# Optimization experiments

Hardware: AMD Instinct MI355X
Metric: run time of the kernel (lower is better)

The kernel has to match this reference:

```python
import jax, jax.numpy as jnp
import numpy as np
import math

IN_F, OUT_F = 512, 512
N_HEADS, N_SPLITS = 32, 4
N = 1024
DELTA_SCALE = 0.1


def setup_inputs() -> dict:
    key = jax.random.key(0)
    k_x, k_h, k_s, k_w = jax.random.split(key, 4)
    stdv = 1.0 / math.sqrt(OUT_F)
    inputs = {
        "input": jax.random.normal(k_x, (N, IN_F), dtype=jnp.float32),
        "head_ix": jax.random.randint(k_h, (N,), 0, N_HEADS, dtype=jnp.int32),
        "split_ix": jax.random.randint(k_s, (N,), 0, N_SPLITS, dtype=jnp.int32),
        # learned parameters (EmbeddingTensor tables)
        "weight": jax.random.uniform(k_w, (N_HEADS, IN_F, OUT_F), dtype=jnp.float32,
                                     minval=-stdv, maxval=stdv),
        "delta_weight": jnp.zeros((N_HEADS * N_SPLITS, IN_F, OUT_F), dtype=jnp.float32),
        "bias": jnp.zeros((N_HEADS, OUT_F), dtype=jnp.float32),
    }
    return inputs


def reference(input, head_ix, split_ix, weight, delta_weight, bias):
    # per-sample weight: base[head] + 0.1 * delta[head * n_splits + split]
    w = weight[head_ix] + delta_weight[head_ix * N_SPLITS + split_ix] * DELTA_SCALE  # [N, in, out]
    # batched vector-matrix multiply + per-head bias
    return jnp.einsum('ab,abc->ac', input, w) + bias[head_ix]  # [N, out]
```

## Files before the change

### kernel.cpp

```cpp
#include <hip/hip_runtime.h>

#define N_SAMP   1024
#define IN_F     512
#define OUT_F    512
#define N_HEADS  32
#define N_SPLITS 4
#define N_GROUPS (N_HEADS * N_SPLITS)
#define DELTA_SCALE 0.1f

#define KSPLIT   8
#define KROWS    (IN_F / KSPLIT)
#define JC       16


__global__ __launch_bounds__(256, 4) void lms_partial(
    const float* __restrict__ X, const int* __restrict__ head_ix,
    const int* __restrict__ split_ix, const float* __restrict__ W,
    const float* __restrict__ D, float* __restrict__ ws)
{
    __shared__ float Xs[JC][KROWS];
    __shared__ int   list[N_SAMP];
    __shared__ int   wsum[4];

    const int b       = blockIdx.x;
    const int logical = (b & 7) * 128 + (b >> 3);
    const int g       = logical >> 3;
    const int kb      = logical & 7;
    const int h       = g >> 2;

    const int tid  = threadIdx.x;
    const int lane = tid & 63;
    const int wave = tid >> 6;

    int run = 0;
    for (int r = 0; r < N_SAMP / 256; ++r) {
        const int i   = r * 256 + tid;
        const int key = head_ix[i] * N_SPLITS + split_ix[i];
        const bool hit = (key == g);
        const unsigned long long m = __ballot(hit);
        if (lane == 0) wsum[wave] = __popcll(m);
        __syncthreads();
        int base = run;
        for (int w = 0; w < 4; ++w)
            if (w < wave) base += wsum[w];
        if (hit)
            list[base + __popcll(m & ((1ULL << lane) - 1ULL))] = i;
        run += wsum[0] + wsum[1] + wsum[2] + wsum[3];
        __syncthreads();
    }
    const int total = run;
    if (total == 0) return;

    const float* wq = W + (size_t)h * (IN_F * OUT_F)
                    + (size_t)(kb * KROWS) * OUT_F + 2 * tid;
    const float* dq = D + (size_t)g * (IN_F * OUT_F)
                    + (size_t)(kb * KROWS) * OUT_F + 2 * tid;

    for (int cb = 0; cb < total; cb += JC) {
        const int nc = min(total - cb, JC);

        __syncthreads();
        {
            const int s  = tid >> 4;
            const int qq = tid & 15;
            float4 v = make_float4(0.f, 0.f, 0.f, 0.f);
            if (s < nc)
                v = *(const float4*)(X + (size_t)list[cb + s] * IN_F
                                     + kb * KROWS + qq * 4);
            *(float4*)(&Xs[s][qq * 4]) = v;
        }
        __syncthreads();

        float2 acc[JC];
#pragma unroll
        for (int j = 0; j < JC; ++j) { acc[j].x = 0.f; acc[j].y = 0.f; }

        float2 wr[2][4], dr[2][4];
#pragma unroll
        for (int f = 0; f < 4; ++f) {
            wr[0][f] = *(const float2*)(wq + (size_t)f * OUT_F);
            dr[0][f] = *(const float2*)(dq + (size_t)f * OUT_F);
        }

        constexpr int NB = KROWS / 4;
#pragma unroll 2
        for (int bt = 0; bt < NB; ++bt) {
            const int cur = bt & 1, nxt = cur ^ 1;
            const int nr = (bt + 1 < NB) ? (bt + 1) * 4 : bt * 4;
#pragma unroll
            for (int f = 0; f < 4; ++f) {
                wr[nxt][f] = *(const float2*)(wq + (size_t)(nr + f) * OUT_F);
                dr[nxt][f] = *(const float2*)(dq + (size_t)(nr + f) * OUT_F);
            }

            float2 rc[4];
#pragma unroll
            for (int f = 0; f < 4; ++f) {
                rc[f].x = wr[cur][f].x + DELTA_SCALE * dr[cur][f].x;
                rc[f].y = wr[cur][f].y + DELTA_SCALE * dr[cur][f].y;
            }

#pragma unroll
            for (int j = 0; j < JC; ++j) {
                const float4 xv = *(const float4*)(&Xs[j][bt * 4]);
                acc[j].x += xv.x * rc[0].x; acc[j].y += xv.x * rc[0].y;
                acc[j].x += xv.y * rc[1].x; acc[j].y += xv.y * rc[1].y;
                acc[j].x += xv.z * rc[2].x; acc[j].y += xv.z * rc[2].y;
                acc[j].x += xv.w * rc[3].x; acc[j].y += xv.w * rc[3].y;
            }
        }

#pragma unroll
        for (int j = 0; j < JC; ++j) {
            if (j < nc) {
                float* op = ws + ((size_t)kb * N_SAMP + list[cb + j]) * OUT_F
                          + 2 * tid;
                *(float2*)op = acc[j];
            }
        }
    }
}

__global__ __launch_bounds__(256, 4) void lms_reduce(
    const float* __restrict__ ws, const int* __restrict__ head_ix,
    const float* __restrict__ bias, float* __restrict__ out)
{
    const int gid = blockIdx.x * 256 + threadIdx.x;
    const int i   = gid >> 7;
    const int c4  = gid & 127;
    const int h   = head_ix[i];

    float4 s = *(const float4*)(bias + (size_t)h * OUT_F + 4 * c4);
#pragma unroll
    for (int kb = 0; kb < KSPLIT; ++kb) {
        const float4 p = *(const float4*)(ws + ((size_t)kb * N_SAMP + i) * OUT_F
                                          + 4 * c4);
        s.x += p.x; s.y += p.y; s.z += p.z; s.w += p.w;
    }
    *(float4*)(out + (size_t)i * OUT_F + 4 * c4) = s;
}

__global__ __launch_bounds__(256, 4) void lms_fused(
    const float* __restrict__ X, const int* __restrict__ head_ix,
    const int* __restrict__ split_ix, const float* __restrict__ W,
    const float* __restrict__ D, const float* __restrict__ bias,
    float* __restrict__ out)
{
    constexpr int J    = 16;
    constexpr int KQ   = 8;
    constexpr int KT   = IN_F / KQ;
    constexpr int NST  = KT / 4;
    constexpr int NOUT = (J * 32) / 256;

    __shared__ float buf[J * IN_F];
    __shared__ int   list[N_SAMP];
    __shared__ int   wsum[4];

    const int g    = blockIdx.y;
    const int h    = g >> 2;
    const int c0   = blockIdx.x * 64;
    const int tid  = threadIdx.x;
    const int c2   = tid & 31;
    const int kq   = tid >> 5;
    const int lane = tid & 63;
    const int wave = tid >> 6;

    int run = 0;
    for (int r = 0; r < N_SAMP / 256; ++r) {
        const int i   = r * 256 + tid;
        const int key = head_ix[i] * N_SPLITS + split_ix[i];
        const bool hit = (key == g);
        const unsigned long long m = __ballot(hit);
        if (lane == 0) wsum[wave] = __popcll(m);
        __syncthreads();
        int base = run;
        for (int w = 0; w < 4; ++w)
            if (w < wave) base += wsum[w];
        if (hit)
            list[base + __popcll(m & ((1ULL << lane) - 1ULL))] = i;
        run += wsum[0] + wsum[1] + wsum[2] + wsum[3];
        __syncthreads();
    }
    const int total = run;
    if (total == 0) return;

    const size_t roff = (size_t)(kq * KT) * OUT_F + c0 + c2 * 2;
    const float* wp = W + (size_t)h * (IN_F * OUT_F) + roff;
    const float* dp = D + (size_t)g * (IN_F * OUT_F) + roff;

    for (int s0 = 0; s0 < total; s0 += J) {
        const int nc = min(total - s0, J);
        __syncthreads();
        for (int i = tid; i < J * (IN_F / 4); i += 256) {
            const int s = i >> 7, q = i & 127;
            float4 v = make_float4(0.f, 0.f, 0.f, 0.f);
            if (s < nc)
                v = *(const float4*)(X + (size_t)list[s0 + s] * IN_F + q * 4);
            *(float4*)(&buf[s * IN_F + q * 4]) = v;
        }
        __syncthreads();

        float2 acc[J];
#pragma unroll
        for (int j = 0; j < J; ++j) { acc[j].x = 0.f; acc[j].y = 0.f; }

        float2 wb[2][4], db[2][4];
#pragma unroll
        for (int u = 0; u < 4; ++u) {
            wb[0][u] = *(const float2*)(wp + (size_t)u * OUT_F);
            db[0][u] = *(const float2*)(dp + (size_t)u * OUT_F);
        }

#pragma unroll 2
        for (int st = 0; st < NST; ++st) {
            const int nx = (st + 1 < NST) ? st + 1 : NST - 1;
            const int nb = (st + 1) & 1, cb = st & 1;
            const float* wn = wp + (size_t)(nx * 4) * OUT_F;
            const float* dn = dp + (size_t)(nx * 4) * OUT_F;
#pragma unroll
            for (int u = 0; u < 4; ++u) {
                wb[nb][u] = *(const float2*)(wn + (size_t)u * OUT_F);
                db[nb][u] = *(const float2*)(dn + (size_t)u * OUT_F);
            }
            float2 rc[4];
#pragma unroll
            for (int u = 0; u < 4; ++u) {
                rc[u].x = wb[cb][u].x + DELTA_SCALE * db[cb][u].x;
                rc[u].y = wb[cb][u].y + DELTA_SCALE * db[cb][u].y;
            }
            const float* xb = &buf[kq * KT + st * 4];
#pragma unroll
            for (int j = 0; j < J; ++j) {
                const float4 xv = *(const float4*)(xb + j * IN_F);
                acc[j].x += xv.x * rc[0].x; acc[j].y += xv.x * rc[0].y;
                acc[j].x += xv.y * rc[1].x; acc[j].y += xv.y * rc[1].y;
                acc[j].x += xv.z * rc[2].x; acc[j].y += xv.z * rc[2].y;
                acc[j].x += xv.w * rc[3].x; acc[j].y += xv.w * rc[3].y;
            }
        }

        __syncthreads();
        float2* Red = (float2*)buf;
#pragma unroll
        for (int j = 0; j < J; ++j)
            Red[(kq * J + j) * 32 + c2] = acc[j];
        __syncthreads();

#pragma unroll
        for (int t = 0; t < NOUT; ++t) {
            const int oi = t * 256 + tid;
            const int j = oi >> 5, cc = oi & 31;
            if (j < nc) {
                float2 s = make_float2(0.f, 0.f);
#pragma unroll
                for (int q = 0; q < KQ; ++q) {
                    const float2 r = Red[(q * J + j) * 32 + cc];
                    s.x += r.x; s.y += r.y;
                }
                const float2 bv =
                    *(const float2*)(bias + (size_t)h * OUT_F + c0 + cc * 2);
                float* op = out + (size_t)list[s0 + j] * OUT_F + c0 + cc * 2;
                float2 res;
                res.x = s.x + bv.x;
                res.y = s.y + bv.y;
                *(float2*)op = res;
            }
        }
    }
}

extern "C" void kernel_launch(void* const* d_in, const int* in_sizes, int n_in,
                              void* d_out, int out_size, void* d_ws, size_t ws_size,
                              hipStream_t stream) {
    const float* X        = (const float*)d_in[0];
    const int*   head_ix  = (const int*)d_in[1];
    const int*   split_ix = (const int*)d_in[2];
    const float* W        = (const float*)d_in[3];
    const float* D        = (const float*)d_in[4];
    const float* bias     = (const float*)d_in[5];
    float*       out      = (float*)d_out;

    const size_t ws_need = (size_t)KSPLIT * N_SAMP * OUT_F * sizeof(float);
    if (ws_size >= ws_need) {
        float* ws = (float*)d_ws;
        lms_partial<<<dim3(N_GROUPS * KSPLIT), 256, 0, stream>>>(
            X, head_ix, split_ix, W, D, ws);
        lms_reduce<<<dim3((N_SAMP * OUT_F / 4) / 256), 256, 0, stream>>>(
            ws, head_ix, bias, out);
    } else {
        dim3 gf(OUT_F / 64, N_GROUPS);
        lms_fused<<<gf, 256, 0, stream>>>(X, head_ix, split_ix, W, D, bias, out);
    }
}
```

Baseline: 269.2 us.

## Widen per-thread output tile to float4 and split K across half-blocks

The partial kernel now has each thread compute four output columns with float4 weight and delta loads. The two halves of a block each cover 64 K rows of a 128-row chunk, so the grid shrinks to 512 blocks. Block indices are remapped so that heads sharing the same K chunk are interleaved, which may improve locality of the base weight in L2. The aim is wider loads and more reuse of each X value from shared memory, at the cost of more registers (launch bounds lowered to 2 blocks per SM) and fewer blocks to hide latency.

Measured after the change: 254.0 us. 1.06x faster.

```diff
diff --git a/kernel.cpp b/kernel.cpp
--- a/kernel.cpp
+++ b/kernel.cpp
@@ -8,27 +8,33 @@
 #define N_GROUPS (N_HEADS * N_SPLITS)
 #define DELTA_SCALE 0.1f
 
-#define KSPLIT   8
-#define KROWS    (IN_F / KSPLIT)
+#define NKB      4
+#define KR2      128
+#define KRH      64
+#define NPLANES  8
 #define JC       16
 
 
-__global__ __launch_bounds__(256, 4) void lms_partial(
+__global__ __launch_bounds__(256, 2) void lms_partial4(
     const float* __restrict__ X, const int* __restrict__ head_ix,
     const int* __restrict__ split_ix, const float* __restrict__ W,
     const float* __restrict__ D, float* __restrict__ ws)
 {
-    __shared__ float Xs[JC][KROWS];
+    __shared__ float Xs[JC][KR2];
     __shared__ int   list[N_SAMP];
     __shared__ int   wsum[4];
 
-    const int b       = blockIdx.x;
-    const int logical = (b & 7) * 128 + (b >> 3);
-    const int g       = logical >> 3;
-    const int kb      = logical & 7;
-    const int h       = g >> 2;
+    const int b   = blockIdx.x;
+    const int x   = b & 7;
+    const int j5  = b >> 3;
+    const int h   = x | ((j5 & 3) << 3);
+    const int s   = (j5 >> 2) & 3;
+    const int kb  = j5 >> 4;
+    const int g   = h * N_SPLITS + s;
 
     const int tid  = threadIdx.x;
+    const int c4   = tid & 127;
+    const int kh   = tid >> 7;
     const int lane = tid & 63;
     const int wave = tid >> 6;
 
@@ -51,71 +57,81 @@
     const int total = run;
     if (total == 0) return;
 
+    const int krow0 = kb * KR2 + kh * KRH;
     const float* wq = W + (size_t)h * (IN_F * OUT_F)
-                    + (size_t)(kb * KROWS) * OUT_F + 2 * tid;
+                    + (size_t)krow0 * OUT_F + 4 * c4;
     const float* dq = D + (size_t)g * (IN_F * OUT_F)
-                    + (size_t)(kb * KROWS) * OUT_F + 2 * tid;
+                    + (size_t)krow0 * OUT_F + 4 * c4;
+    const int plane = kb * 2 + kh;
 
     for (int cb = 0; cb < total; cb += JC) {
         const int nc = min(total - cb, JC);
 
         __syncthreads();
-        {
-            const int s  = tid >> 4;
-            const int qq = tid & 15;
+        for (int f = 0; f < 2; ++f) {
+            const int fid = f * 256 + tid;
+            const int ss = fid >> 5, qq = fid & 31;
             float4 v = make_float4(0.f, 0.f, 0.f, 0.f);
-            if (s < nc)
-                v = *(const float4*)(X + (size_t)list[cb + s] * IN_F
-                                     + kb * KROWS + qq * 4);
-            *(float4*)(&Xs[s][qq * 4]) = v;
-        }
-        __syncthreads();
-
-        float2 acc[JC];
-#pragma unroll
-        for (int j = 0; j < JC; ++j) { acc[j].x = 0.f; acc[j].y = 0.f; }
-
-        float2 wr[2][4], dr[2][4];
+            if (ss < nc)
+                v = *(const float4*)(X + (size_t)list[cb + ss] * IN_F
+                                     + kb * KR2 + qq * 4);
+            *(float4*)(&Xs[ss][qq * 4]) = v;
+        }
+        __syncthreads();
+
+        float4 acc[JC];
+#pragma unroll
+        for (int j = 0; j < JC; ++j)
+            acc[j] = make_float4(0.f, 0.f, 0.f, 0.f);
+
+        float4 wr[2][4], dr[2][4];
 #pragma unroll
         for (int f = 0; f < 4; ++f) {
-            wr[0][f] = *(const float2*)(wq + (size_t)f * OUT_F);
-            dr[0][f] = *(const float2*)(dq + (size_t)f * OUT_F);
-        }
-
-        constexpr int NB = KROWS / 4;
+            wr[0][f] = *(const float4*)(wq + (size_t)f * OUT_F);
+            dr[0][f] = *(const float4*)(dq + (size_t)f * OUT_F);
+        }
+
+        constexpr int NB = KRH / 4;
 #pragma unroll 2
         for (int bt = 0; bt < NB; ++bt) {
             const int cur = bt & 1, nxt = cur ^ 1;
             const int nr = (bt + 1 < NB) ? (bt + 1) * 4 : bt * 4;
 #pragma unroll
             for (int f = 0; f < 4; ++f) {
-                wr[nxt][f] = *(const float2*)(wq + (size_t)(nr + f) * OUT_F);
-                dr[nxt][f] = *(const float2*)(dq + (size_t)(nr + f) * OUT_F);
-            }
-
-            float2 rc[4];
+                wr[nxt][f] = *(const float4*)(wq + (size_t)(nr + f) * OUT_F);
+                dr[nxt][f] = *(const float4*)(dq + (size_t)(nr + f) * OUT_F);
+            }
+
+            float4 rc[4];
 #pragma unroll
             for (int f = 0; f < 4; ++f) {
                 rc[f].x = wr[cur][f].x + DELTA_SCALE * dr[cur][f].x;
                 rc[f].y = wr[cur][f].y + DELTA_SCALE * dr[cur][f].y;
+                rc[f].z = wr[cur][f].z + DELTA_SCALE * dr[cur][f].z;
+                rc[f].w = wr[cur][f].w + DELTA_SCALE * dr[cur][f].w;
             }
 
 #pragma unroll
             for (int j = 0; j < JC; ++j) {
-                const float4 xv = *(const float4*)(&Xs[j][bt * 4]);
+                const float4 xv =
+                    *(const float4*)(&Xs[j][kh * KRH + bt * 4]);
                 acc[j].x += xv.x * rc[0].x; acc[j].y += xv.x * rc[0].y;
+                acc[j].z += xv.x * rc[0].z; acc[j].w += xv.x * rc[0].w;
                 acc[j].x += xv.y * rc[1].x; acc[j].y += xv.y * rc[1].y;
+                acc[j].z += xv.y * rc[1].z; acc[j].w += xv.y * rc[1].w;
                 acc[j].x += xv.z * rc[2].x; acc[j].y += xv.z * rc[2].y;
+                acc[j].z += xv.z * rc[2].z; acc[j].w += xv.z * rc[2].w;
                 acc[j].x += xv.w * rc[3].x; acc[j].y += xv.w * rc[3].y;
+                acc[j].z += xv.w * rc[3].z; acc[j].w += xv.w * rc[3].w;
             }
         }
 
 #pragma unroll
         for (int j = 0; j < JC; ++j) {
             if (j < nc) {
-                float* op = ws + ((size_t)kb * N_SAMP + list[cb + j]) * OUT_F
-                          + 2 * tid;
-                *(float2*)op = acc[j];
+                float* op = ws + ((size_t)plane * N_SAMP + list[cb + j]) * OUT_F
+                          + 4 * c4;
+                *(float4*)op = acc[j];
             }
         }
     }
@@ -132,10 +148,10 @@
 
     float4 s = *(const float4*)(bias + (size_t)h * OUT_F + 4 * c4);
 #pragma unroll
-    for (int kb = 0; kb < KSPLIT; ++kb) {
-        const float4 p = *(const float4*)(ws + ((size_t)kb * N_SAMP + i) * OUT_F
+    for (int p = 0; p < NPLANES; ++p) {
+        const float4 v = *(const float4*)(ws + ((size_t)p * N_SAMP + i) * OUT_F
                                           + 4 * c4);
-        s.x += p.x; s.y += p.y; s.z += p.z; s.w += p.w;
+        s.x += v.x; s.y += v.y; s.z += v.z; s.w += v.w;
     }
     *(float4*)(out + (size_t)i * OUT_F + 4 * c4) = s;
 }
@@ -280,10 +296,10 @@
     const float* bias     = (const float*)d_in[5];
     float*       out      = (float*)d_out;
 
-    const size_t ws_need = (size_t)KSPLIT * N_SAMP * OUT_F * sizeof(float);
+    const size_t ws_need = (size_t)NPLANES * N_SAMP * OUT_F * sizeof(float);
     if (ws_size >= ws_need) {
         float* ws = (float*)d_ws;
-        lms_partial<<<dim3(N_GROUPS * KSPLIT), 256, 0, stream>>>(
+        lms_partial4<<<dim3(N_GROUPS * NKB), 256, 0, stream>>>(
             X, head_ix, split_ix, W, D, ws);
         lms_reduce<<<dim3((N_SAMP * OUT_F / 4) / 256), 256, 0, stream>>>(
             ws, head_ix, bias, out);
```
